# Optimization experiments

Hardware: AMD Instinct MI355X
Metric: run time of the kernel (lower is better)

The kernel has to match this reference:

```python
import jax, jax.numpy as jnp
import numpy as np

N_NODES = 100000
N_EDGES = 1250000
IN_DIM = 6
HID = 64


def gcn_conv(x, W, b, src, dst, deg_inv_sqrt):
    # x: [N, F_in] -> [N, F_out]; symmetric-normalized aggregation with self-loops
    h = x @ W  # [N, F_out]
    norm = deg_inv_sqrt[src] * deg_inv_sqrt[dst]  # [E]
    msg = h[src] * norm[:, None]                  # gather + scale, [E, F_out]
    agg = jax.ops.segment_sum(msg, dst, num_segments=x.shape[0])
    # self-loop contribution: norm = deg_inv_sqrt[i]^2 = 1/deg[i]
    out = agg + h * (deg_inv_sqrt ** 2)[:, None] + b
    return out


def setup_inputs() -> dict:
    key = jax.random.key(0)
    ks = jax.random.split(key, 8)
    x = jax.random.normal(ks[0], (N_NODES, IN_DIM), dtype=jnp.float32)
    edge_index = jax.random.randint(ks[1], (2, N_EDGES), 0, N_NODES, dtype=jnp.int64)
    s1 = 1.0 / np.sqrt(IN_DIM)
    s2 = 1.0 / np.sqrt(HID)
    W1 = jax.random.uniform(ks[2], (IN_DIM, HID), jnp.float32, -s1, s1)
    b1 = jnp.zeros((HID,), jnp.float32)
    W2 = jax.random.uniform(ks[3], (HID, HID), jnp.float32, -s2, s2)
    b2 = jnp.zeros((HID,), jnp.float32)
    Wfc = jax.random.uniform(ks[4], (HID, 1), jnp.float32, -s2, s2)
    bfc = jnp.zeros((1,), jnp.float32)
    return {"x": x, "edge_index": edge_index, "W1": W1, "b1": b1,
            "W2": W2, "b2": b2, "Wfc": Wfc, "bfc": bfc}


def reference(x, edge_index, W1, b1, W2, b2, Wfc, bfc):
    src, dst = edge_index[0], edge_index[1]
    n = x.shape[0]
    # degree with self-loops (GCN default): in-degree at destination + 1
    deg = jax.ops.segment_sum(jnp.ones((src.shape[0],), x.dtype), dst, num_segments=n) + 1.0
    deg_inv_sqrt = jax.lax.rsqrt(deg)
    h = gcn_conv(x, W1, b1, src, dst, deg_inv_sqrt)
    h = jax.nn.relu(h)
    h = gcn_conv(h, W2, b2, src, dst, deg_inv_sqrt)
    g = h.mean(axis=0)              # [HID] graph readout
    out = jax.nn.sigmoid(g @ Wfc + bfc)  # [1]
    return out
```

## Files before the change

### kernel.cpp

```cpp
#include <hip/hip_runtime.h>
#include <math.h>

#define N_NODES 100000
#define N_EDGES 1250000
#define IN_DIM 6
#define HID 64

#define BIN_SHIFT 8
#define BIN_NODES 256
#define NBIN 391
#define A_BLOCKS 250
#define EPB (N_EDGES / A_BLOCKS)
#define CAP 4096
#define SOFF (NBIN * CAP)

__device__ inline float lo16(unsigned u) { return __uint_as_float(u << 16); }
__device__ inline float hi16(unsigned u) { return __uint_as_float(u & 0xffff0000u); }
__device__ inline unsigned short f2bf(float f) {
    unsigned u = __float_as_uint(f);
    u += 0x7FFFu + ((u >> 16) & 1u);
    return (unsigned short)(u >> 16);
}
__device__ inline unsigned pack2(float a, float b) {
    return (unsigned)f2bf(a) | ((unsigned)f2bf(b) << 16);
}

__global__ __launch_bounds__(1024) void binFill(const int* __restrict__ src,
                                                const int* __restrict__ dst,
                                                int* __restrict__ cnt,
                                                unsigned* __restrict__ rec) {
    __shared__ int lc[NBIN];
    __shared__ int scv[NBIN];
    __shared__ int lb[NBIN];
    __shared__ int lbase[NBIN];
    __shared__ unsigned ldsRec[EPB];
    __shared__ int ldsPos[EPB];

    int t = threadIdx.x;
    int base = blockIdx.x * EPB;

    int4 dA = *(const int4*)&dst[base + t * 4];
    int4 sA = *(const int4*)&src[base + t * 4];
    const int TB = (EPB - 4096) / 4;
    bool hasB = (t < TB);
    int4 dB = make_int4(0, 0, 0, 0), sB = make_int4(0, 0, 0, 0);
    if (hasB) {
        dB = *(const int4*)&dst[base + 4096 + t * 4];
        sB = *(const int4*)&src[base + 4096 + t * 4];
    }

#define HIST4(v4) do {                                  \
        atomicAdd(&lc[(v4).x >> BIN_SHIFT], 1);         \
        atomicAdd(&lc[(v4).y >> BIN_SHIFT], 1);         \
        atomicAdd(&lc[(v4).z >> BIN_SHIFT], 1);         \
        atomicAdd(&lc[(v4).w >> BIN_SHIFT], 1);         \
    } while (0)

#define SCAT1(key, val) do {                                                  \
        int b_ = (key) >> BIN_SHIFT;                                          \
        int loc_ = lbase[b_] + atomicAdd(&lc[b_], 1);                         \
        loc_ = min(loc_, EPB - 1);                                            \
        ldsRec[loc_] = ((unsigned)((key) & (BIN_NODES - 1)) << 17)            \
                     | (unsigned)(val);                                       \
        ldsPos[loc_] = lb[b_] + (loc_ - lbase[b_]);                           \
    } while (0)

#define SCAT4(k4, v4) do {                  \
        SCAT1((k4).x, (v4).x);              \
        SCAT1((k4).y, (v4).y);              \
        SCAT1((k4).z, (v4).z);              \
        SCAT1((k4).w, (v4).w);              \
    } while (0)

#define WRITEOUT() do {                                                       \
        for (int i = t; i < EPB; i += 1024) {                                 \
            unsigned p_ = (unsigned)ldsPos[i];                                \
            if (p_ < (unsigned)(2 * SOFF)) rec[p_] = ldsRec[i];               \
        }                                                                     \
    } while (0)

    if (t < NBIN) lc[t] = 0;
    __syncthreads();
    HIST4(dA);
    if (hasB) HIST4(dB);
    __syncthreads();
    if (t < NBIN) {
        int c = lc[t];
        scv[t] = c;
        lc[t] = 0;
        int off = (c > 0) ? atomicAdd(&cnt[t], c) : 0;
        lb[t] = t * CAP + off;
    }
    __syncthreads();
    if (t < 64) {
        int carry = 0;
#pragma unroll
        for (int cb = 0; cb < NBIN; cb += 64) {
            int idx = cb + t;
            int c = (idx < NBIN) ? scv[idx] : 0;
            int v = c;
#pragma unroll
            for (int off = 1; off < 64; off <<= 1) {
                int u = __shfl_up(v, off, 64);
                if (t >= off) v += u;
            }
            if (idx < NBIN) lbase[idx] = carry + v - c;
            carry += __shfl(v, 63, 64);
        }
    }
    __syncthreads();
    SCAT4(dA, sA);
    if (hasB) SCAT4(dB, sB);
    __syncthreads();
    WRITEOUT();
    __syncthreads();

    if (t < NBIN) lc[t] = 0;
    __syncthreads();
    HIST4(sA);
    if (hasB) HIST4(sB);
    __syncthreads();
    if (t < NBIN) {
        int c = lc[t];
        scv[t] = c;
        lc[t] = 0;
        int off = (c > 0) ? atomicAdd(&cnt[NBIN + t], c) : 0;
        lb[t] = SOFF + t * CAP + off;
    }
    __syncthreads();
    if (t < 64) {
        int carry = 0;
#pragma unroll
        for (int cb = 0; cb < NBIN; cb += 64) {
            int idx = cb + t;
            int c = (idx < NBIN) ? scv[idx] : 0;
            int v = c;
#pragma unroll
            for (int off = 1; off < 64; off <<= 1) {
                int u = __shfl_up(v, off, 64);
                if (t >= off) v += u;
            }
            if (idx < NBIN) lbase[idx] = carry + v - c;
            carry += __shfl(v, 63, 64);
        }
    }
    __syncthreads();
    SCAT4(sA, dA);
    if (hasB) SCAT4(sB, dB);
    __syncthreads();
    WRITEOUT();

#undef HIST4
#undef SCAT1
#undef SCAT4
#undef WRITEOUT
}

__global__ __launch_bounds__(1024) void disXH(const unsigned* __restrict__ rec,
                                              const int* __restrict__ cnt,
                                              const float* __restrict__ x,
                                              int* __restrict__ deg,
                                              float* __restrict__ dis,
                                              uint4* __restrict__ xpad) {
    __shared__ int histS[4][BIN_NODES];
    int t = threadIdx.x, g = t >> 8;
    if (t < 4 * BIN_NODES) ((int*)histS)[t] = 0;
    __syncthreads();
    int bin = blockIdx.x;
    int beg = bin * CAP, end = beg + cnt[bin];
    for (int j = beg + t; j < end; j += 1024) atomicAdd(&histS[g][rec[j] >> 17], 1);
    __syncthreads();
    if (t < BIN_NODES) {
        int n = (bin << BIN_SHIFT) + t;
        if (n < N_NODES) {
            int h = histS[0][t] + histS[1][t] + histS[2][t] + histS[3][t];
            deg[n] = h;
            float d = rsqrtf((float)h + 1.0f);
            dis[n] = d;
            float2 xa = *(const float2*)&x[n * IN_DIM + 0];
            float2 xb = *(const float2*)&x[n * IN_DIM + 2];
            float2 xc = *(const float2*)&x[n * IN_DIM + 4];
            uint4 u;
            u.x = pack2(xa.x * d, xa.y * d);
            u.y = pack2(xb.x * d, xb.y * d);
            u.z = pack2(xc.x * d, xc.y * d);
            u.w = 0;
            xpad[n] = u;
        }
    }
}

__global__ __launch_bounds__(1024) void aggW(const unsigned* __restrict__ rec,
                                             const int* __restrict__ cnt,
                                             const int* __restrict__ deg,
                                             const float* __restrict__ dis,
                                             const uint4* __restrict__ xpad,
                                             const float* __restrict__ W1,
                                             const float* __restrict__ b1,
                                             float* __restrict__ vsum) {
    __shared__ unsigned srcL[CAP];
    __shared__ float wlS[4][BIN_NODES];
    __shared__ int degL[BIN_NODES];
    __shared__ int startS[BIN_NODES];
    __shared__ int cur[BIN_NODES];
    __shared__ int sc[BIN_NODES];
    __shared__ float sAll[BIN_NODES][8];
    __shared__ float w1s[IN_DIM * HID];
    __shared__ float b1s[HID];
    __shared__ float vpart[HID];
    int t = threadIdx.x, g = t >> 8;
    int bin = blockIdx.x;

    if (t < 4 * BIN_NODES) ((float*)wlS)[t] = 0.f;
    if (t < IN_DIM * HID) w1s[t] = W1[t];
    if (t >= 1024 - HID) { int c = t - (1024 - HID); b1s[c] = b1[c]; vpart[c] = 0.f; }
    __syncthreads();

    {
        int beg = SOFF + bin * CAP, end = beg + cnt[NBIN + bin];
        for (int j = beg + t; j < end; j += 1024) {
            unsigned r = rec[j];
            atomicAdd(&wlS[g][r >> 17], dis[r & 131071u]);
        }
    }
    __syncthreads();

    if (t < BIN_NODES) {
        int n = (bin << BIN_SHIFT) + t;
        int h = (n < N_NODES) ? deg[n] : 0;
        degL[t] = h;
        sc[t] = h;
        float d = (n < N_NODES) ? rsqrtf((float)h + 1.0f) : 0.f;
        float wloc = wlS[0][t] + wlS[1][t] + wlS[2][t] + wlS[3][t];
        sAll[t][6] = d;
        sAll[t][7] = (n < N_NODES) ? d * (wloc + d) : 0.f;
    }
    __syncthreads();
    for (int off = 1; off < BIN_NODES; off <<= 1) {
        int add = 0;
        if (t < BIN_NODES && t >= off) add = sc[t - off];
        __syncthreads();
        if (t < BIN_NODES) sc[t] += add;
        __syncthreads();
    }
    if (t < BIN_NODES) {
        int st = sc[t] - degL[t];
        startS[t] = st;
        cur[t] = st;
    }
    __syncthreads();

    {
        int beg = bin * CAP, end = beg + cnt[bin];
        for (int j = beg + t; j < end; j += 1024) {
            unsigned r = rec[j];
            int pos = atomicAdd(&cur[r >> 17], 1);
            if (pos < CAP) srcL[pos] = r & 131071u;
        }
    }
    __syncthreads();

    {
        int node = t >> 2, sub = t & 3;
        int st = startS[node], cn = degL[node];
        int lim = min(st + cn, CAP);
        float s0 = 0.f, s1 = 0.f, s2 = 0.f, s3 = 0.f, s4 = 0.f, s5 = 0.f;
        for (int k = st + sub; k < lim; k += 4) {
            uint4 px = xpad[srcL[k]];
            s0 += lo16(px.x); s1 += hi16(px.x);
            s2 += lo16(px.y); s3 += hi16(px.y);
            s4 += lo16(px.z); s5 += hi16(px.z);
        }
        s0 += __shfl_xor(s0, 1, 64); s0 += __shfl_xor(s0, 2, 64);
        s1 += __shfl_xor(s1, 1, 64); s1 += __shfl_xor(s1, 2, 64);
        s2 += __shfl_xor(s2, 1, 64); s2 += __shfl_xor(s2, 2, 64);
        s3 += __shfl_xor(s3, 1, 64); s3 += __shfl_xor(s3, 2, 64);
        s4 += __shfl_xor(s4, 1, 64); s4 += __shfl_xor(s4, 2, 64);
        s5 += __shfl_xor(s5, 1, 64); s5 += __shfl_xor(s5, 2, 64);
        if (sub == 0) {
            int n = (bin << BIN_SHIFT) + node;
            if (n < N_NODES) {
                uint4 px = xpad[n];
                s0 += lo16(px.x); s1 += hi16(px.x);
                s2 += lo16(px.y); s3 += hi16(px.y);
                s4 += lo16(px.z); s5 += hi16(px.z);
            }
            sAll[node][0] = s0; sAll[node][1] = s1; sAll[node][2] = s2;
            sAll[node][3] = s3; sAll[node][4] = s4; sAll[node][5] = s5;
        }
    }
    __syncthreads();

    {
        int c = t & 63, grp = t >> 6;
        float v = 0.f;
#pragma unroll
        for (int i = 0; i < 16; ++i) {
            int node = grp * 16 + i;
            float d = sAll[node][6], cw = sAll[node][7];
            float a = sAll[node][0] * w1s[0 * HID + c]
                    + sAll[node][1] * w1s[1 * HID + c]
                    + sAll[node][2] * w1s[2 * HID + c]
                    + sAll[node][3] * w1s[3 * HID + c]
                    + sAll[node][4] * w1s[4 * HID + c]
                    + sAll[node][5] * w1s[5 * HID + c];
            v += cw * fmaxf(d * a + b1s[c], 0.f);
        }
        atomicAdd(&vpart[c], v);
    }
    __syncthreads();
    if (t < HID) atomicAdd(&vsum[t], vpart[t]);
}

__global__ void finalK(const float* __restrict__ vsum, const float* __restrict__ W2,
                       const float* __restrict__ b2, const float* __restrict__ Wfc,
                       const float* __restrict__ bfc, float* __restrict__ out) {
    __shared__ float vL[HID];
    int t = threadIdx.x;
    vL[t] = vsum[t] * (1.0f / N_NODES);
    __syncthreads();
    float g = b2[t];
    for (int k = 0; k < HID; ++k) g += vL[k] * W2[k * HID + t];
    float z = g * Wfc[t];
    for (int off = 32; off > 0; off >>= 1) z += __shfl_down(z, off, 64);
    if (t == 0) out[0] = 1.0f / (1.0f + expf(-(z + bfc[0])));
}

extern "C" void kernel_launch(void* const* d_in, const int* in_sizes, int n_in,
                              void* d_out, int out_size, void* d_ws, size_t ws_size,
                              hipStream_t stream) {
    const float* x   = (const float*)d_in[0];
    const int*   ei  = (const int*)d_in[1];
    const float* W1  = (const float*)d_in[2];
    const float* b1  = (const float*)d_in[3];
    const float* W2  = (const float*)d_in[4];
    const float* b2  = (const float*)d_in[5];
    const float* Wfc = (const float*)d_in[6];
    const float* bfc = (const float*)d_in[7];
    const int* src = ei;
    const int* dst = ei + N_EDGES;

    char* ws = (char*)d_ws;
    size_t off = 0;
    auto alloc = (+[](char* base, size_t* o, size_t bytes) {
        char* p = base + *o;
        *o += (bytes + 255) & ~(size_t)255;
        return p;
    });
    int*      cnt  = (int*)     alloc(ws, &off, (size_t)2 * NBIN * 4);
    float*    vsum = (float*)   alloc(ws, &off, 64 * 4);
    uint4*    xpad = (uint4*)   alloc(ws, &off, (size_t)N_NODES * 16);
    float*    dis  = (float*)   alloc(ws, &off, (size_t)N_NODES * 4);
    int*      deg  = (int*)     alloc(ws, &off, (size_t)N_NODES * 4);
    unsigned* rec  = (unsigned*)alloc(ws, &off, (size_t)2 * SOFF * 4);

    hipMemsetAsync(cnt, 0, ((size_t)2 * NBIN * 4 + 255 & ~(size_t)255) + 64 * 4, stream);

    binFill<<<A_BLOCKS, 1024, 0, stream>>>(src, dst, cnt, rec);
    disXH<<<NBIN, 1024, 0, stream>>>(rec, cnt, x, deg, dis, xpad);
    aggW<<<NBIN, 1024, 0, stream>>>(rec, cnt, deg, dis, xpad, W1, b1, vsum);
    finalK<<<1, 64, 0, stream>>>(vsum, W2, b2, Wfc, bfc, (float*)d_out);
}
```

Baseline: 124.0 us.

## Drop source-binned edge copy; push-scatter dis weights via global atomics

Removes the second binning pass by source node, which halves the record buffer and skips one histogram, scan, scatter and writeout in binFill. The per-source sum of destination dis values is now computed in the degree kernel: each dst-bin block stages its records in LDS and does a global atomicAdd of dis[dst] into wsum[src]. aggW then reads wsum instead of accumulating it from source-binned records. The trade is about 1.25M scattered global float atomics in place of the LDS-local accumulation, plus a larger memset that now also clears wsum.

```diff
diff --git a/kernel.cpp b/kernel.cpp
--- a/kernel.cpp
+++ b/kernel.cpp
@@ -70,13 +70,6 @@
         SCAT1((k4).y, (v4).y);              \
         SCAT1((k4).z, (v4).z);              \
         SCAT1((k4).w, (v4).w);              \
-    } while (0)
-
-#define WRITEOUT() do {                                                       \
-        for (int i = t; i < EPB; i += 1024) {                                 \
-            unsigned p_ = (unsigned)ldsPos[i];                                \
-            if (p_ < (unsigned)(2 * SOFF)) rec[p_] = ldsRec[i];               \
-        }                                                                     \
     } while (0)
 
     if (t < NBIN) lc[t] = 0;
@@ -112,71 +105,45 @@
     SCAT4(dA, sA);
     if (hasB) SCAT4(dB, sB);
     __syncthreads();
-    WRITEOUT();
-    __syncthreads();
-
-    if (t < NBIN) lc[t] = 0;
-    __syncthreads();
-    HIST4(sA);
-    if (hasB) HIST4(sB);
-    __syncthreads();
-    if (t < NBIN) {
-        int c = lc[t];
-        scv[t] = c;
-        lc[t] = 0;
-        int off = (c > 0) ? atomicAdd(&cnt[NBIN + t], c) : 0;
-        lb[t] = SOFF + t * CAP + off;
-    }
-    __syncthreads();
-    if (t < 64) {
-        int carry = 0;
-#pragma unroll
-        for (int cb = 0; cb < NBIN; cb += 64) {
-            int idx = cb + t;
-            int c = (idx < NBIN) ? scv[idx] : 0;
-            int v = c;
-#pragma unroll
-            for (int off = 1; off < 64; off <<= 1) {
-                int u = __shfl_up(v, off, 64);
-                if (t >= off) v += u;
-            }
-            if (idx < NBIN) lbase[idx] = carry + v - c;
-            carry += __shfl(v, 63, 64);
-        }
-    }
-    __syncthreads();
-    SCAT4(sA, dA);
-    if (hasB) SCAT4(sB, dB);
-    __syncthreads();
-    WRITEOUT();
+    for (int i = t; i < EPB; i += 1024) {
+        unsigned p = (unsigned)ldsPos[i];
+        if (p < (unsigned)SOFF) rec[p] = ldsRec[i];
+    }
 
 #undef HIST4
 #undef SCAT1
 #undef SCAT4
-#undef WRITEOUT
-}
-
-__global__ __launch_bounds__(1024) void disXH(const unsigned* __restrict__ rec,
+}
+
+__global__ __launch_bounds__(1024) void disXS(const unsigned* __restrict__ rec,
                                               const int* __restrict__ cnt,
                                               const float* __restrict__ x,
                                               int* __restrict__ deg,
-                                              float* __restrict__ dis,
-                                              uint4* __restrict__ xpad) {
+                                              uint4* __restrict__ xpad,
+                                              float* __restrict__ wsum) {
+    __shared__ unsigned stage[CAP];
     __shared__ int histS[4][BIN_NODES];
+    __shared__ float disL[BIN_NODES];
     int t = threadIdx.x, g = t >> 8;
     if (t < 4 * BIN_NODES) ((int*)histS)[t] = 0;
     __syncthreads();
     int bin = blockIdx.x;
-    int beg = bin * CAP, end = beg + cnt[bin];
-    for (int j = beg + t; j < end; j += 1024) atomicAdd(&histS[g][rec[j] >> 17], 1);
+    int beg = bin * CAP;
+    int cn = cnt[bin];
+    if (cn > CAP) cn = CAP;
+    for (int j = t; j < cn; j += 1024) {
+        unsigned r = rec[beg + j];
+        stage[j] = r;
+        atomicAdd(&histS[g][r >> 17], 1);
+    }
     __syncthreads();
     if (t < BIN_NODES) {
         int n = (bin << BIN_SHIFT) + t;
+        float d = 0.f;
         if (n < N_NODES) {
             int h = histS[0][t] + histS[1][t] + histS[2][t] + histS[3][t];
             deg[n] = h;
-            float d = rsqrtf((float)h + 1.0f);
-            dis[n] = d;
+            d = rsqrtf((float)h + 1.0f);
             float2 xa = *(const float2*)&x[n * IN_DIM + 0];
             float2 xb = *(const float2*)&x[n * IN_DIM + 2];
             float2 xc = *(const float2*)&x[n * IN_DIM + 4];
@@ -187,19 +154,24 @@
             u.w = 0;
             xpad[n] = u;
         }
+        disL[t] = d;
+    }
+    __syncthreads();
+    for (int j = t; j < cn; j += 1024) {
+        unsigned r = stage[j];
+        atomicAdd(&wsum[r & 131071u], disL[r >> 17]);
     }
 }
 
 __global__ __launch_bounds__(1024) void aggW(const unsigned* __restrict__ rec,
                                              const int* __restrict__ cnt,
                                              const int* __restrict__ deg,
-                                             const float* __restrict__ dis,
+                                             const float* __restrict__ wsum,
                                              const uint4* __restrict__ xpad,
                                              const float* __restrict__ W1,
                                              const float* __restrict__ b1,
                                              float* __restrict__ vsum) {
     __shared__ unsigned srcL[CAP];
-    __shared__ float wlS[4][BIN_NODES];
     __shared__ int degL[BIN_NODES];
     __shared__ int startS[BIN_NODES];
     __shared__ int cur[BIN_NODES];
@@ -208,22 +180,11 @@
     __shared__ float w1s[IN_DIM * HID];
     __shared__ float b1s[HID];
     __shared__ float vpart[HID];
-    int t = threadIdx.x, g = t >> 8;
+    int t = threadIdx.x;
     int bin = blockIdx.x;
 
-    if (t < 4 * BIN_NODES) ((float*)wlS)[t] = 0.f;
     if (t < IN_DIM * HID) w1s[t] = W1[t];
     if (t >= 1024 - HID) { int c = t - (1024 - HID); b1s[c] = b1[c]; vpart[c] = 0.f; }
-    __syncthreads();
-
-    {
-        int beg = SOFF + bin * CAP, end = beg + cnt[NBIN + bin];
-        for (int j = beg + t; j < end; j += 1024) {
-            unsigned r = rec[j];
-            atomicAdd(&wlS[g][r >> 17], dis[r & 131071u]);
-        }
-    }
-    __syncthreads();
 
     if (t < BIN_NODES) {
         int n = (bin << BIN_SHIFT) + t;
@@ -231,7 +192,7 @@
         degL[t] = h;
         sc[t] = h;
         float d = (n < N_NODES) ? rsqrtf((float)h + 1.0f) : 0.f;
-        float wloc = wlS[0][t] + wlS[1][t] + wlS[2][t] + wlS[3][t];
+        float wloc = (n < N_NODES) ? wsum[n] : 0.f;
         sAll[t][6] = d;
         sAll[t][7] = (n < N_NODES) ? d * (wloc + d) : 0.f;
     }
@@ -347,17 +308,17 @@
         *o += (bytes + 255) & ~(size_t)255;
         return p;
     });
-    int*      cnt  = (int*)     alloc(ws, &off, (size_t)2 * NBIN * 4);
+    int*      cnt  = (int*)     alloc(ws, &off, (size_t)NBIN * 4);
     float*    vsum = (float*)   alloc(ws, &off, 64 * 4);
+    float*    wsum = (float*)   alloc(ws, &off, (size_t)N_NODES * 4);
     uint4*    xpad = (uint4*)   alloc(ws, &off, (size_t)N_NODES * 16);
-    float*    dis  = (float*)   alloc(ws, &off, (size_t)N_NODES * 4);
     int*      deg  = (int*)     alloc(ws, &off, (size_t)N_NODES * 4);
-    unsigned* rec  = (unsigned*)alloc(ws, &off, (size_t)2 * SOFF * 4);
-
-    hipMemsetAsync(cnt, 0, ((size_t)2 * NBIN * 4 + 255 & ~(size_t)255) + 64 * 4, stream);
+    unsigned* rec  = (unsigned*)alloc(ws, &off, (size_t)SOFF * 4);
+
+    hipMemsetAsync(cnt, 0, (size_t)((char*)xpad - (char*)cnt), stream);
 
     binFill<<<A_BLOCKS, 1024, 0, stream>>>(src, dst, cnt, rec);
-    disXH<<<NBIN, 1024, 0, stream>>>(rec, cnt, x, deg, dis, xpad);
-    aggW<<<NBIN, 1024, 0, stream>>>(rec, cnt, deg, dis, xpad, W1, b1, vsum);
+    disXS<<<NBIN, 1024, 0, stream>>>(rec, cnt, x, deg, xpad, wsum);
+    aggW<<<NBIN, 1024, 0, stream>>>(rec, cnt, deg, wsum, xpad, W1, b1, vsum);
     finalK<<<1, 64, 0, stream>>>(vsum, W2, b2, Wfc, bfc, (float*)d_out);
 }
```

New measurement: 176.9 us. 42.6% more time.

## Fuse all four kernels into one cooperative persistent kernel with grid syncs

Applied to the files above, without the earlier changes.

Replaces the four separate launches (bin fill, degree/xpad, aggregation, final) with a single cooperative kernel of 256 blocks. The phases are separated by grid.sync, and later phases loop over the 391 bins in a grid-stride loop. Shared memory is overlaid through a union of the per-phase layouts. The aim is to remove the launch gaps and tail idle time between kernels, in exchange for grid-sync overhead, fewer blocks than bins in the bin phases (some blocks handle two bins), and idle blocks during the final step.

```diff
diff --git a/kernel.cpp b/kernel.cpp
--- a/kernel.cpp
+++ b/kernel.cpp
@@ -1,5 +1,8 @@
 #include <hip/hip_runtime.h>
+#include <hip/hip_cooperative_groups.h>
 #include <math.h>
+
+namespace cg = cooperative_groups;
 
 #define N_NODES 100000
 #define N_EDGES 1250000
@@ -13,6 +16,7 @@
 #define EPB (N_EDGES / A_BLOCKS)
 #define CAP 4096
 #define SOFF (NBIN * CAP)
+#define GRID_B 256
 
 __device__ inline float lo16(unsigned u) { return __uint_as_float(u << 16); }
 __device__ inline float hi16(unsigned u) { return __uint_as_float(u & 0xffff0000u); }
@@ -25,305 +29,300 @@
     return (unsigned)f2bf(a) | ((unsigned)f2bf(b) << 16);
 }
 
-__global__ __launch_bounds__(1024) void binFill(const int* __restrict__ src,
-                                                const int* __restrict__ dst,
-                                                int* __restrict__ cnt,
-                                                unsigned* __restrict__ rec) {
-    __shared__ int lc[NBIN];
-    __shared__ int scv[NBIN];
-    __shared__ int lb[NBIN];
-    __shared__ int lbase[NBIN];
-    __shared__ unsigned ldsRec[EPB];
-    __shared__ int ldsPos[EPB];
-
+struct P1 {
+    int lc[NBIN];
+    int scv[NBIN];
+    int lb[NBIN];
+    int lbase[NBIN];
+    unsigned ldsRec[EPB];
+    int ldsPos[EPB];
+};
+struct P23 {
+    unsigned srcL[CAP];
+    union { int hist[4][BIN_NODES]; float wl[4][BIN_NODES]; } h;
+    int degL[BIN_NODES];
+    int startS[BIN_NODES];
+    int cur[BIN_NODES];
+    int sc[BIN_NODES];
+    float sAll[BIN_NODES][8];
+    float w1s[IN_DIM * HID];
+    float b1s[HID];
+    float vpart[HID];
+};
+
+__global__ __launch_bounds__(1024) void fused(
+    const int* __restrict__ src, const int* __restrict__ dst,
+    const float* __restrict__ x,
+    const float* __restrict__ W1, const float* __restrict__ b1,
+    const float* __restrict__ W2, const float* __restrict__ b2,
+    const float* __restrict__ Wfc, const float* __restrict__ bfc,
+    int* __restrict__ cnt, unsigned* __restrict__ rec,
+    int* __restrict__ deg, float* __restrict__ dis,
+    uint4* __restrict__ xpad, float* __restrict__ vsum,
+    float* __restrict__ out)
+{
+    __shared__ union { P1 a; P23 b; } S;
+    cg::grid_group grid = cg::this_grid();
     int t = threadIdx.x;
-    int base = blockIdx.x * EPB;
-
-    int4 dA = *(const int4*)&dst[base + t * 4];
-    int4 sA = *(const int4*)&src[base + t * 4];
-    const int TB = (EPB - 4096) / 4;
-    bool hasB = (t < TB);
-    int4 dB = make_int4(0, 0, 0, 0), sB = make_int4(0, 0, 0, 0);
-    if (hasB) {
-        dB = *(const int4*)&dst[base + 4096 + t * 4];
-        sB = *(const int4*)&src[base + 4096 + t * 4];
-    }
-
-#define HIST4(v4) do {                                  \
-        atomicAdd(&lc[(v4).x >> BIN_SHIFT], 1);         \
-        atomicAdd(&lc[(v4).y >> BIN_SHIFT], 1);         \
-        atomicAdd(&lc[(v4).z >> BIN_SHIFT], 1);         \
-        atomicAdd(&lc[(v4).w >> BIN_SHIFT], 1);         \
-    } while (0)
+
+    if (blockIdx.x < A_BLOCKS) {
+        int base = blockIdx.x * EPB;
+        int4 dA = *(const int4*)&dst[base + t * 4];
+        int4 sA = *(const int4*)&src[base + t * 4];
+        const int TB = (EPB - 4096) / 4;
+        bool hasB = (t < TB);
+        int4 dB = make_int4(0, 0, 0, 0), sB = make_int4(0, 0, 0, 0);
+        if (hasB) {
+            dB = *(const int4*)&dst[base + 4096 + t * 4];
+            sB = *(const int4*)&src[base + 4096 + t * 4];
+        }
+
+#define HIST4(v4) do {                                      \
+            atomicAdd(&S.a.lc[(v4).x >> BIN_SHIFT], 1);     \
+            atomicAdd(&S.a.lc[(v4).y >> BIN_SHIFT], 1);     \
+            atomicAdd(&S.a.lc[(v4).z >> BIN_SHIFT], 1);     \
+            atomicAdd(&S.a.lc[(v4).w >> BIN_SHIFT], 1);     \
+        } while (0)
 
 #define SCAT1(key, val) do {                                                  \
-        int b_ = (key) >> BIN_SHIFT;                                          \
-        int loc_ = lbase[b_] + atomicAdd(&lc[b_], 1);                         \
-        loc_ = min(loc_, EPB - 1);                                            \
-        ldsRec[loc_] = ((unsigned)((key) & (BIN_NODES - 1)) << 17)            \
-                     | (unsigned)(val);                                       \
-        ldsPos[loc_] = lb[b_] + (loc_ - lbase[b_]);                           \
-    } while (0)
+            int b_ = (key) >> BIN_SHIFT;                                      \
+            int loc_ = S.a.lbase[b_] + atomicAdd(&S.a.lc[b_], 1);             \
+            loc_ = min(loc_, EPB - 1);                                        \
+            S.a.ldsRec[loc_] = ((unsigned)((key) & (BIN_NODES - 1)) << 17)    \
+                             | (unsigned)(val);                               \
+            S.a.ldsPos[loc_] = S.a.lb[b_] + (loc_ - S.a.lbase[b_]);           \
+        } while (0)
 
 #define SCAT4(k4, v4) do {                  \
-        SCAT1((k4).x, (v4).x);              \
-        SCAT1((k4).y, (v4).y);              \
-        SCAT1((k4).z, (v4).z);              \
-        SCAT1((k4).w, (v4).w);              \
-    } while (0)
+            SCAT1((k4).x, (v4).x);          \
+            SCAT1((k4).y, (v4).y);          \
+            SCAT1((k4).z, (v4).z);          \
+            SCAT1((k4).w, (v4).w);          \
+        } while (0)
+
+#define WAVE_SCAN() do {                                                      \
+            if (t < 64) {                                                     \
+                int carry = 0;                                                \
+                for (int cb = 0; cb < NBIN; cb += 64) {                       \
+                    int idx = cb + t;                                         \
+                    int c = (idx < NBIN) ? S.a.scv[idx] : 0;                  \
+                    int v = c;                                                \
+                    for (int off = 1; off < 64; off <<= 1) {                  \
+                        int u = __shfl_up(v, off, 64);                        \
+                        if (t >= off) v += u;                                 \
+                    }                                                         \
+                    if (idx < NBIN) S.a.lbase[idx] = carry + v - c;           \
+                    carry += __shfl(v, 63, 64);                               \
+                }                                                             \
+            }                                                                 \
+        } while (0)
 
 #define WRITEOUT() do {                                                       \
-        for (int i = t; i < EPB; i += 1024) {                                 \
-            unsigned p_ = (unsigned)ldsPos[i];                                \
-            if (p_ < (unsigned)(2 * SOFF)) rec[p_] = ldsRec[i];               \
-        }                                                                     \
-    } while (0)
-
-    if (t < NBIN) lc[t] = 0;
-    __syncthreads();
-    HIST4(dA);
-    if (hasB) HIST4(dB);
-    __syncthreads();
-    if (t < NBIN) {
-        int c = lc[t];
-        scv[t] = c;
-        lc[t] = 0;
-        int off = (c > 0) ? atomicAdd(&cnt[t], c) : 0;
-        lb[t] = t * CAP + off;
-    }
-    __syncthreads();
-    if (t < 64) {
-        int carry = 0;
-#pragma unroll
-        for (int cb = 0; cb < NBIN; cb += 64) {
-            int idx = cb + t;
-            int c = (idx < NBIN) ? scv[idx] : 0;
-            int v = c;
-#pragma unroll
-            for (int off = 1; off < 64; off <<= 1) {
-                int u = __shfl_up(v, off, 64);
-                if (t >= off) v += u;
-            }
-            if (idx < NBIN) lbase[idx] = carry + v - c;
-            carry += __shfl(v, 63, 64);
-        }
-    }
-    __syncthreads();
-    SCAT4(dA, sA);
-    if (hasB) SCAT4(dB, sB);
-    __syncthreads();
-    WRITEOUT();
-    __syncthreads();
-
-    if (t < NBIN) lc[t] = 0;
-    __syncthreads();
-    HIST4(sA);
-    if (hasB) HIST4(sB);
-    __syncthreads();
-    if (t < NBIN) {
-        int c = lc[t];
-        scv[t] = c;
-        lc[t] = 0;
-        int off = (c > 0) ? atomicAdd(&cnt[NBIN + t], c) : 0;
-        lb[t] = SOFF + t * CAP + off;
-    }
-    __syncthreads();
-    if (t < 64) {
-        int carry = 0;
-#pragma unroll
-        for (int cb = 0; cb < NBIN; cb += 64) {
-            int idx = cb + t;
-            int c = (idx < NBIN) ? scv[idx] : 0;
-            int v = c;
-#pragma unroll
-            for (int off = 1; off < 64; off <<= 1) {
-                int u = __shfl_up(v, off, 64);
-                if (t >= off) v += u;
-            }
-            if (idx < NBIN) lbase[idx] = carry + v - c;
-            carry += __shfl(v, 63, 64);
-        }
-    }
-    __syncthreads();
-    SCAT4(sA, dA);
-    if (hasB) SCAT4(sB, dB);
-    __syncthreads();
-    WRITEOUT();
+            for (int i = t; i < EPB; i += 1024) {                             \
+                unsigned p_ = (unsigned)S.a.ldsPos[i];                        \
+                if (p_ < (unsigned)(2 * SOFF)) rec[p_] = S.a.ldsRec[i];       \
+            }                                                                 \
+        } while (0)
+
+        if (t < NBIN) S.a.lc[t] = 0;
+        __syncthreads();
+        HIST4(dA);
+        if (hasB) HIST4(dB);
+        __syncthreads();
+        if (t < NBIN) {
+            int c = S.a.lc[t];
+            S.a.scv[t] = c;
+            S.a.lc[t] = 0;
+            int off = (c > 0) ? atomicAdd(&cnt[t], c) : 0;
+            S.a.lb[t] = t * CAP + off;
+        }
+        __syncthreads();
+        WAVE_SCAN();
+        __syncthreads();
+        SCAT4(dA, sA);
+        if (hasB) SCAT4(dB, sB);
+        __syncthreads();
+        WRITEOUT();
+        __syncthreads();
+
+        if (t < NBIN) S.a.lc[t] = 0;
+        __syncthreads();
+        HIST4(sA);
+        if (hasB) HIST4(sB);
+        __syncthreads();
+        if (t < NBIN) {
+            int c = S.a.lc[t];
+            S.a.scv[t] = c;
+            S.a.lc[t] = 0;
+            int off = (c > 0) ? atomicAdd(&cnt[NBIN + t], c) : 0;
+            S.a.lb[t] = SOFF + t * CAP + off;
+        }
+        __syncthreads();
+        WAVE_SCAN();
+        __syncthreads();
+        SCAT4(sA, dA);
+        if (hasB) SCAT4(sB, dB);
+        __syncthreads();
+        WRITEOUT();
 
 #undef HIST4
 #undef SCAT1
 #undef SCAT4
+#undef WAVE_SCAN
 #undef WRITEOUT
-}
-
-__global__ __launch_bounds__(1024) void disXH(const unsigned* __restrict__ rec,
-                                              const int* __restrict__ cnt,
-                                              const float* __restrict__ x,
-                                              int* __restrict__ deg,
-                                              float* __restrict__ dis,
-                                              uint4* __restrict__ xpad) {
-    __shared__ int histS[4][BIN_NODES];
-    int t = threadIdx.x, g = t >> 8;
-    if (t < 4 * BIN_NODES) ((int*)histS)[t] = 0;
-    __syncthreads();
-    int bin = blockIdx.x;
-    int beg = bin * CAP, end = beg + cnt[bin];
-    for (int j = beg + t; j < end; j += 1024) atomicAdd(&histS[g][rec[j] >> 17], 1);
-    __syncthreads();
-    if (t < BIN_NODES) {
-        int n = (bin << BIN_SHIFT) + t;
-        if (n < N_NODES) {
-            int h = histS[0][t] + histS[1][t] + histS[2][t] + histS[3][t];
-            deg[n] = h;
-            float d = rsqrtf((float)h + 1.0f);
-            dis[n] = d;
-            float2 xa = *(const float2*)&x[n * IN_DIM + 0];
-            float2 xb = *(const float2*)&x[n * IN_DIM + 2];
-            float2 xc = *(const float2*)&x[n * IN_DIM + 4];
-            uint4 u;
-            u.x = pack2(xa.x * d, xa.y * d);
-            u.y = pack2(xb.x * d, xb.y * d);
-            u.z = pack2(xc.x * d, xc.y * d);
-            u.w = 0;
-            xpad[n] = u;
-        }
-    }
-}
-
-__global__ __launch_bounds__(1024) void aggW(const unsigned* __restrict__ rec,
-                                             const int* __restrict__ cnt,
-                                             const int* __restrict__ deg,
-                                             const float* __restrict__ dis,
-                                             const uint4* __restrict__ xpad,
-                                             const float* __restrict__ W1,
-                                             const float* __restrict__ b1,
-                                             float* __restrict__ vsum) {
-    __shared__ unsigned srcL[CAP];
-    __shared__ float wlS[4][BIN_NODES];
-    __shared__ int degL[BIN_NODES];
-    __shared__ int startS[BIN_NODES];
-    __shared__ int cur[BIN_NODES];
-    __shared__ int sc[BIN_NODES];
-    __shared__ float sAll[BIN_NODES][8];
-    __shared__ float w1s[IN_DIM * HID];
-    __shared__ float b1s[HID];
-    __shared__ float vpart[HID];
-    int t = threadIdx.x, g = t >> 8;
-    int bin = blockIdx.x;
-
-    if (t < 4 * BIN_NODES) ((float*)wlS)[t] = 0.f;
-    if (t < IN_DIM * HID) w1s[t] = W1[t];
-    if (t >= 1024 - HID) { int c = t - (1024 - HID); b1s[c] = b1[c]; vpart[c] = 0.f; }
-    __syncthreads();
-
-    {
-        int beg = SOFF + bin * CAP, end = beg + cnt[NBIN + bin];
-        for (int j = beg + t; j < end; j += 1024) {
-            unsigned r = rec[j];
-            atomicAdd(&wlS[g][r >> 17], dis[r & 131071u]);
-        }
-    }
-    __syncthreads();
-
-    if (t < BIN_NODES) {
-        int n = (bin << BIN_SHIFT) + t;
-        int h = (n < N_NODES) ? deg[n] : 0;
-        degL[t] = h;
-        sc[t] = h;
-        float d = (n < N_NODES) ? rsqrtf((float)h + 1.0f) : 0.f;
-        float wloc = wlS[0][t] + wlS[1][t] + wlS[2][t] + wlS[3][t];
-        sAll[t][6] = d;
-        sAll[t][7] = (n < N_NODES) ? d * (wloc + d) : 0.f;
-    }
-    __syncthreads();
-    for (int off = 1; off < BIN_NODES; off <<= 1) {
-        int add = 0;
-        if (t < BIN_NODES && t >= off) add = sc[t - off];
-        __syncthreads();
-        if (t < BIN_NODES) sc[t] += add;
-        __syncthreads();
-    }
-    if (t < BIN_NODES) {
-        int st = sc[t] - degL[t];
-        startS[t] = st;
-        cur[t] = st;
-    }
-    __syncthreads();
-
-    {
-        int beg = bin * CAP, end = beg + cnt[bin];
-        for (int j = beg + t; j < end; j += 1024) {
-            unsigned r = rec[j];
-            int pos = atomicAdd(&cur[r >> 17], 1);
-            if (pos < CAP) srcL[pos] = r & 131071u;
-        }
-    }
-    __syncthreads();
-
-    {
-        int node = t >> 2, sub = t & 3;
-        int st = startS[node], cn = degL[node];
-        int lim = min(st + cn, CAP);
-        float s0 = 0.f, s1 = 0.f, s2 = 0.f, s3 = 0.f, s4 = 0.f, s5 = 0.f;
-        for (int k = st + sub; k < lim; k += 4) {
-            uint4 px = xpad[srcL[k]];
-            s0 += lo16(px.x); s1 += hi16(px.x);
-            s2 += lo16(px.y); s3 += hi16(px.y);
-            s4 += lo16(px.z); s5 += hi16(px.z);
-        }
-        s0 += __shfl_xor(s0, 1, 64); s0 += __shfl_xor(s0, 2, 64);
-        s1 += __shfl_xor(s1, 1, 64); s1 += __shfl_xor(s1, 2, 64);
-        s2 += __shfl_xor(s2, 1, 64); s2 += __shfl_xor(s2, 2, 64);
-        s3 += __shfl_xor(s3, 1, 64); s3 += __shfl_xor(s3, 2, 64);
-        s4 += __shfl_xor(s4, 1, 64); s4 += __shfl_xor(s4, 2, 64);
-        s5 += __shfl_xor(s5, 1, 64); s5 += __shfl_xor(s5, 2, 64);
-        if (sub == 0) {
-            int n = (bin << BIN_SHIFT) + node;
+    }
+    grid.sync();
+
+    if (t < IN_DIM * HID) S.b.w1s[t] = W1[t];
+    if (t >= 1024 - HID) {
+        int c = t - (1024 - HID);
+        S.b.b1s[c] = b1[c];
+        S.b.vpart[c] = 0.f;
+    }
+
+    for (int bin = (int)blockIdx.x; bin < NBIN; bin += GRID_B) {
+        if (t < 4 * BIN_NODES) ((int*)S.b.h.hist)[t] = 0;
+        __syncthreads();
+        int beg = bin * CAP;
+        int cn = cnt[bin]; if (cn > CAP) cn = CAP;
+        int g = t >> 8;
+        for (int j = t; j < cn; j += 1024)
+            atomicAdd(&S.b.h.hist[g][rec[beg + j] >> 17], 1);
+        __syncthreads();
+        if (t < BIN_NODES) {
+            int n = (bin << BIN_SHIFT) + t;
             if (n < N_NODES) {
-                uint4 px = xpad[n];
+                int h = S.b.h.hist[0][t] + S.b.h.hist[1][t]
+                      + S.b.h.hist[2][t] + S.b.h.hist[3][t];
+                deg[n] = h;
+                float d = rsqrtf((float)h + 1.0f);
+                dis[n] = d;
+                float2 xa = *(const float2*)&x[n * IN_DIM + 0];
+                float2 xb = *(const float2*)&x[n * IN_DIM + 2];
+                float2 xc = *(const float2*)&x[n * IN_DIM + 4];
+                uint4 u;
+                u.x = pack2(xa.x * d, xa.y * d);
+                u.y = pack2(xb.x * d, xb.y * d);
+                u.z = pack2(xc.x * d, xc.y * d);
+                u.w = 0;
+                xpad[n] = u;
+            }
+        }
+        __syncthreads();
+    }
+    grid.sync();
+
+    for (int bin = (int)blockIdx.x; bin < NBIN; bin += GRID_B) {
+        if (t < 4 * BIN_NODES) ((float*)S.b.h.wl)[t] = 0.f;
+        __syncthreads();
+        {
+            int beg2 = SOFF + bin * CAP;
+            int cn2 = cnt[NBIN + bin]; if (cn2 > CAP) cn2 = CAP;
+            int g = t >> 8;
+            for (int j = t; j < cn2; j += 1024) {
+                unsigned r = rec[beg2 + j];
+                atomicAdd(&S.b.h.wl[g][r >> 17], dis[r & 131071u]);
+            }
+        }
+        __syncthreads();
+        if (t < BIN_NODES) {
+            int n = (bin << BIN_SHIFT) + t;
+            int h = (n < N_NODES) ? deg[n] : 0;
+            S.b.degL[t] = h;
+            S.b.sc[t] = h;
+            float d = (n < N_NODES) ? rsqrtf((float)h + 1.0f) : 0.f;
+            float wloc = S.b.h.wl[0][t] + S.b.h.wl[1][t]
+                       + S.b.h.wl[2][t] + S.b.h.wl[3][t];
+            S.b.sAll[t][6] = d;
+            S.b.sAll[t][7] = (n < N_NODES) ? d * (wloc + d) : 0.f;
+        }
+        __syncthreads();
+        for (int off = 1; off < BIN_NODES; off <<= 1) {
+            int add = 0;
+            if (t < BIN_NODES && t >= off) add = S.b.sc[t - off];
+            __syncthreads();
+            if (t < BIN_NODES) S.b.sc[t] += add;
+            __syncthreads();
+        }
+        if (t < BIN_NODES) {
+            int st = S.b.sc[t] - S.b.degL[t];
+            S.b.startS[t] = st;
+            S.b.cur[t] = st;
+        }
+        __syncthreads();
+        {
+            int beg = bin * CAP;
+            int cn = cnt[bin]; if (cn > CAP) cn = CAP;
+            for (int j = t; j < cn; j += 1024) {
+                unsigned r = rec[beg + j];
+                int pos = atomicAdd(&S.b.cur[r >> 17], 1);
+                if (pos < CAP) S.b.srcL[pos] = r & 131071u;
+            }
+        }
+        __syncthreads();
+        {
+            int node = t >> 2, sub = t & 3;
+            int st = S.b.startS[node], cnD = S.b.degL[node];
+            int lim = min(st + cnD, CAP);
+            float s0 = 0.f, s1 = 0.f, s2 = 0.f, s3 = 0.f, s4 = 0.f, s5 = 0.f;
+            for (int k = st + sub; k < lim; k += 4) {
+                uint4 px = xpad[S.b.srcL[k]];
                 s0 += lo16(px.x); s1 += hi16(px.x);
                 s2 += lo16(px.y); s3 += hi16(px.y);
                 s4 += lo16(px.z); s5 += hi16(px.z);
             }
-            sAll[node][0] = s0; sAll[node][1] = s1; sAll[node][2] = s2;
-            sAll[node][3] = s3; sAll[node][4] = s4; sAll[node][5] = s5;
-        }
-    }
-    __syncthreads();
-
-    {
-        int c = t & 63, grp = t >> 6;
-        float v = 0.f;
+            s0 += __shfl_xor(s0, 1, 64); s0 += __shfl_xor(s0, 2, 64);
+            s1 += __shfl_xor(s1, 1, 64); s1 += __shfl_xor(s1, 2, 64);
+            s2 += __shfl_xor(s2, 1, 64); s2 += __shfl_xor(s2, 2, 64);
+            s3 += __shfl_xor(s3, 1, 64); s3 += __shfl_xor(s3, 2, 64);
+            s4 += __shfl_xor(s4, 1, 64); s4 += __shfl_xor(s4, 2, 64);
+            s5 += __shfl_xor(s5, 1, 64); s5 += __shfl_xor(s5, 2, 64);
+            if (sub == 0) {
+                int n = (bin << BIN_SHIFT) + node;
+                if (n < N_NODES) {
+                    uint4 px = xpad[n];
+                    s0 += lo16(px.x); s1 += hi16(px.x);
+                    s2 += lo16(px.y); s3 += hi16(px.y);
+                    s4 += lo16(px.z); s5 += hi16(px.z);
+                }
+                S.b.sAll[node][0] = s0; S.b.sAll[node][1] = s1;
+                S.b.sAll[node][2] = s2; S.b.sAll[node][3] = s3;
+                S.b.sAll[node][4] = s4; S.b.sAll[node][5] = s5;
+            }
+        }
+        __syncthreads();
+        {
+            int c = t & 63, grp = t >> 6;
+            float v = 0.f;
 #pragma unroll
-        for (int i = 0; i < 16; ++i) {
-            int node = grp * 16 + i;
-            float d = sAll[node][6], cw = sAll[node][7];
-            float a = sAll[node][0] * w1s[0 * HID + c]
-                    + sAll[node][1] * w1s[1 * HID + c]
-                    + sAll[node][2] * w1s[2 * HID + c]
-                    + sAll[node][3] * w1s[3 * HID + c]
-                    + sAll[node][4] * w1s[4 * HID + c]
-                    + sAll[node][5] * w1s[5 * HID + c];
-            v += cw * fmaxf(d * a + b1s[c], 0.f);
-        }
-        atomicAdd(&vpart[c], v);
-    }
-    __syncthreads();
-    if (t < HID) atomicAdd(&vsum[t], vpart[t]);
-}
-
-__global__ void finalK(const float* __restrict__ vsum, const float* __restrict__ W2,
-                       const float* __restrict__ b2, const float* __restrict__ Wfc,
-                       const float* __restrict__ bfc, float* __restrict__ out) {
-    __shared__ float vL[HID];
-    int t = threadIdx.x;
-    vL[t] = vsum[t] * (1.0f / N_NODES);
-    __syncthreads();
-    float g = b2[t];
-    for (int k = 0; k < HID; ++k) g += vL[k] * W2[k * HID + t];
-    float z = g * Wfc[t];
-    for (int off = 32; off > 0; off >>= 1) z += __shfl_down(z, off, 64);
-    if (t == 0) out[0] = 1.0f / (1.0f + expf(-(z + bfc[0])));
+            for (int i = 0; i < 16; ++i) {
+                int node = grp * 16 + i;
+                float d = S.b.sAll[node][6], cw = S.b.sAll[node][7];
+                float a = S.b.sAll[node][0] * S.b.w1s[0 * HID + c]
+                        + S.b.sAll[node][1] * S.b.w1s[1 * HID + c]
+                        + S.b.sAll[node][2] * S.b.w1s[2 * HID + c]
+                        + S.b.sAll[node][3] * S.b.w1s[3 * HID + c]
+                        + S.b.sAll[node][4] * S.b.w1s[4 * HID + c]
+                        + S.b.sAll[node][5] * S.b.w1s[5 * HID + c];
+                v += cw * fmaxf(d * a + S.b.b1s[c], 0.f);
+            }
+            atomicAdd(&S.b.vpart[c], v);
+        }
+        __syncthreads();
+    }
+    if (t < HID) atomicAdd(&vsum[t], S.b.vpart[t]);
+    grid.sync();
+
+    if (blockIdx.x == 0 && t < 64) {
+        float vv = vsum[t] * (1.0f / N_NODES);
+        float gacc = b2[t];
+#pragma unroll 8
+        for (int k = 0; k < HID; ++k)
+            gacc += __shfl(vv, k, 64) * W2[k * HID + t];
+        float z = gacc * Wfc[t];
+        for (int off = 32; off > 0; off >>= 1) z += __shfl_down(z, off, 64);
+        if (t == 0) out[0] = 1.0f / (1.0f + expf(-(z + bfc[0])));
+    }
 }
 
 extern "C" void kernel_launch(void* const* d_in, const int* in_sizes, int n_in,
@@ -349,15 +348,21 @@
     });
     int*      cnt  = (int*)     alloc(ws, &off, (size_t)2 * NBIN * 4);
     float*    vsum = (float*)   alloc(ws, &off, 64 * 4);
+    int*      deg  = (int*)     alloc(ws, &off, (size_t)N_NODES * 4);
+    float*    dis  = (float*)   alloc(ws, &off, (size_t)N_NODES * 4);
     uint4*    xpad = (uint4*)   alloc(ws, &off, (size_t)N_NODES * 16);
-    float*    dis  = (float*)   alloc(ws, &off, (size_t)N_NODES * 4);
-    int*      deg  = (int*)     alloc(ws, &off, (size_t)N_NODES * 4);
     unsigned* rec  = (unsigned*)alloc(ws, &off, (size_t)2 * SOFF * 4);
 
-    hipMemsetAsync(cnt, 0, ((size_t)2 * NBIN * 4 + 255 & ~(size_t)255) + 64 * 4, stream);
-
-    binFill<<<A_BLOCKS, 1024, 0, stream>>>(src, dst, cnt, rec);
-    disXH<<<NBIN, 1024, 0, stream>>>(rec, cnt, x, deg, dis, xpad);
-    aggW<<<NBIN, 1024, 0, stream>>>(rec, cnt, deg, dis, xpad, W1, b1, vsum);
-    finalK<<<1, 64, 0, stream>>>(vsum, W2, b2, Wfc, bfc, (float*)d_out);
+    hipMemsetAsync(cnt, 0, (size_t)((char*)deg - (char*)cnt), stream);
+
+    float* outp = (float*)d_out;
+    void* args[] = {
+        (void*)&src, (void*)&dst, (void*)&x,
+        (void*)&W1, (void*)&b1, (void*)&W2, (void*)&b2,
+        (void*)&Wfc, (void*)&bfc,
+        (void*)&cnt, (void*)&rec, (void*)&deg, (void*)&dis,
+        (void*)&xpad, (void*)&vsum, (void*)&outp
+    };
+    hipLaunchCooperativeKernel((void*)fused, dim3(GRID_B), dim3(1024),
+                               args, 0, stream);
 }
```

Measured after the change: 242.4 us. 95.4% more time.

## Halve block size of disXH/aggW and use wave-level shuffle scan for offsets

Applied to the files above, without the earlier changes.

Reduces disXH and aggW from 1024 to 512 threads per block, with 2 histogram copies instead of 4 and 2 lanes per node instead of 4 in the gather. The 256-entry prefix scan of node degrees moves from a shared-memory scan with many __syncthreads to a single wavefront doing __shfl_up scans in four 64-wide chunks. Bin counts are clamped to CAP and the workspace buffers are reordered so the memset size is computed from pointers. The aim is lower barrier cost and smaller blocks so more blocks fit per CU, at the cost of fewer threads per bin.

```diff
diff --git a/kernel.cpp b/kernel.cpp
--- a/kernel.cpp
+++ b/kernel.cpp
@@ -156,24 +156,25 @@
 #undef WRITEOUT
 }
 
-__global__ __launch_bounds__(1024) void disXH(const unsigned* __restrict__ rec,
-                                              const int* __restrict__ cnt,
-                                              const float* __restrict__ x,
-                                              int* __restrict__ deg,
-                                              float* __restrict__ dis,
-                                              uint4* __restrict__ xpad) {
-    __shared__ int histS[4][BIN_NODES];
+__global__ __launch_bounds__(512) void disXH(const unsigned* __restrict__ rec,
+                                             const int* __restrict__ cnt,
+                                             const float* __restrict__ x,
+                                             int* __restrict__ deg,
+                                             float* __restrict__ dis,
+                                             uint4* __restrict__ xpad) {
+    __shared__ int histS[2][BIN_NODES];
     int t = threadIdx.x, g = t >> 8;
-    if (t < 4 * BIN_NODES) ((int*)histS)[t] = 0;
+    if (t < 2 * BIN_NODES) ((int*)histS)[t] = 0;
     __syncthreads();
     int bin = blockIdx.x;
-    int beg = bin * CAP, end = beg + cnt[bin];
-    for (int j = beg + t; j < end; j += 1024) atomicAdd(&histS[g][rec[j] >> 17], 1);
+    int beg = bin * CAP;
+    int cn = cnt[bin]; if (cn > CAP) cn = CAP;
+    for (int j = t; j < cn; j += 512) atomicAdd(&histS[g][rec[beg + j] >> 17], 1);
     __syncthreads();
     if (t < BIN_NODES) {
         int n = (bin << BIN_SHIFT) + t;
         if (n < N_NODES) {
-            int h = histS[0][t] + histS[1][t] + histS[2][t] + histS[3][t];
+            int h = histS[0][t] + histS[1][t];
             deg[n] = h;
             float d = rsqrtf((float)h + 1.0f);
             dis[n] = d;
@@ -190,20 +191,19 @@
     }
 }
 
-__global__ __launch_bounds__(1024) void aggW(const unsigned* __restrict__ rec,
-                                             const int* __restrict__ cnt,
-                                             const int* __restrict__ deg,
-                                             const float* __restrict__ dis,
-                                             const uint4* __restrict__ xpad,
-                                             const float* __restrict__ W1,
-                                             const float* __restrict__ b1,
-                                             float* __restrict__ vsum) {
+__global__ __launch_bounds__(512) void aggW(const unsigned* __restrict__ rec,
+                                            const int* __restrict__ cnt,
+                                            const int* __restrict__ deg,
+                                            const float* __restrict__ dis,
+                                            const uint4* __restrict__ xpad,
+                                            const float* __restrict__ W1,
+                                            const float* __restrict__ b1,
+                                            float* __restrict__ vsum) {
     __shared__ unsigned srcL[CAP];
-    __shared__ float wlS[4][BIN_NODES];
+    __shared__ float wlS[2][BIN_NODES];
     __shared__ int degL[BIN_NODES];
     __shared__ int startS[BIN_NODES];
     __shared__ int cur[BIN_NODES];
-    __shared__ int sc[BIN_NODES];
     __shared__ float sAll[BIN_NODES][8];
     __shared__ float w1s[IN_DIM * HID];
     __shared__ float b1s[HID];
@@ -211,15 +211,16 @@
     int t = threadIdx.x, g = t >> 8;
     int bin = blockIdx.x;
 
-    if (t < 4 * BIN_NODES) ((float*)wlS)[t] = 0.f;
+    if (t < 2 * BIN_NODES) ((float*)wlS)[t] = 0.f;
     if (t < IN_DIM * HID) w1s[t] = W1[t];
-    if (t >= 1024 - HID) { int c = t - (1024 - HID); b1s[c] = b1[c]; vpart[c] = 0.f; }
+    if (t >= 512 - HID) { int c = t - (512 - HID); b1s[c] = b1[c]; vpart[c] = 0.f; }
     __syncthreads();
 
     {
-        int beg = SOFF + bin * CAP, end = beg + cnt[NBIN + bin];
-        for (int j = beg + t; j < end; j += 1024) {
-            unsigned r = rec[j];
+        int beg = SOFF + bin * CAP;
+        int cn = cnt[NBIN + bin]; if (cn > CAP) cn = CAP;
+        for (int j = t; j < cn; j += 512) {
+            unsigned r = rec[beg + j];
             atomicAdd(&wlS[g][r >> 17], dis[r & 131071u]);
         }
     }
@@ -229,31 +230,37 @@
         int n = (bin << BIN_SHIFT) + t;
         int h = (n < N_NODES) ? deg[n] : 0;
         degL[t] = h;
-        sc[t] = h;
         float d = (n < N_NODES) ? rsqrtf((float)h + 1.0f) : 0.f;
-        float wloc = wlS[0][t] + wlS[1][t] + wlS[2][t] + wlS[3][t];
+        float wloc = wlS[0][t] + wlS[1][t];
         sAll[t][6] = d;
         sAll[t][7] = (n < N_NODES) ? d * (wloc + d) : 0.f;
     }
     __syncthreads();
-    for (int off = 1; off < BIN_NODES; off <<= 1) {
-        int add = 0;
-        if (t < BIN_NODES && t >= off) add = sc[t - off];
-        __syncthreads();
-        if (t < BIN_NODES) sc[t] += add;
-        __syncthreads();
-    }
-    if (t < BIN_NODES) {
-        int st = sc[t] - degL[t];
-        startS[t] = st;
-        cur[t] = st;
+    if (t < 64) {
+        int carry = 0;
+#pragma unroll
+        for (int cb = 0; cb < BIN_NODES; cb += 64) {
+            int idx = cb + t;
+            int c = degL[idx];
+            int v = c;
+#pragma unroll
+            for (int off = 1; off < 64; off <<= 1) {
+                int u = __shfl_up(v, off, 64);
+                if (t >= off) v += u;
+            }
+            int st = carry + v - c;
+            startS[idx] = st;
+            cur[idx] = st;
+            carry += __shfl(v, 63, 64);
+        }
     }
     __syncthreads();
 
     {
-        int beg = bin * CAP, end = beg + cnt[bin];
-        for (int j = beg + t; j < end; j += 1024) {
-            unsigned r = rec[j];
+        int beg = bin * CAP;
+        int cn = cnt[bin]; if (cn > CAP) cn = CAP;
+        for (int j = t; j < cn; j += 512) {
+            unsigned r = rec[beg + j];
             int pos = atomicAdd(&cur[r >> 17], 1);
             if (pos < CAP) srcL[pos] = r & 131071u;
         }
@@ -261,22 +268,22 @@
     __syncthreads();
 
     {
-        int node = t >> 2, sub = t & 3;
+        int node = t >> 1, sub = t & 1;
         int st = startS[node], cn = degL[node];
         int lim = min(st + cn, CAP);
         float s0 = 0.f, s1 = 0.f, s2 = 0.f, s3 = 0.f, s4 = 0.f, s5 = 0.f;
-        for (int k = st + sub; k < lim; k += 4) {
+        for (int k = st + sub; k < lim; k += 2) {
             uint4 px = xpad[srcL[k]];
             s0 += lo16(px.x); s1 += hi16(px.x);
             s2 += lo16(px.y); s3 += hi16(px.y);
             s4 += lo16(px.z); s5 += hi16(px.z);
         }
-        s0 += __shfl_xor(s0, 1, 64); s0 += __shfl_xor(s0, 2, 64);
-        s1 += __shfl_xor(s1, 1, 64); s1 += __shfl_xor(s1, 2, 64);
-        s2 += __shfl_xor(s2, 1, 64); s2 += __shfl_xor(s2, 2, 64);
-        s3 += __shfl_xor(s3, 1, 64); s3 += __shfl_xor(s3, 2, 64);
-        s4 += __shfl_xor(s4, 1, 64); s4 += __shfl_xor(s4, 2, 64);
-        s5 += __shfl_xor(s5, 1, 64); s5 += __shfl_xor(s5, 2, 64);
+        s0 += __shfl_xor(s0, 1, 64);
+        s1 += __shfl_xor(s1, 1, 64);
+        s2 += __shfl_xor(s2, 1, 64);
+        s3 += __shfl_xor(s3, 1, 64);
+        s4 += __shfl_xor(s4, 1, 64);
+        s5 += __shfl_xor(s5, 1, 64);
         if (sub == 0) {
             int n = (bin << BIN_SHIFT) + node;
             if (n < N_NODES) {
@@ -295,8 +302,8 @@
         int c = t & 63, grp = t >> 6;
         float v = 0.f;
 #pragma unroll
-        for (int i = 0; i < 16; ++i) {
-            int node = grp * 16 + i;
+        for (int i = 0; i < 32; ++i) {
+            int node = grp * 32 + i;
             float d = sAll[node][6], cw = sAll[node][7];
             float a = sAll[node][0] * w1s[0 * HID + c]
                     + sAll[node][1] * w1s[1 * HID + c]
@@ -349,15 +356,15 @@
     });
     int*      cnt  = (int*)     alloc(ws, &off, (size_t)2 * NBIN * 4);
     float*    vsum = (float*)   alloc(ws, &off, 64 * 4);
+    int*      deg  = (int*)     alloc(ws, &off, (size_t)N_NODES * 4);
+    float*    dis  = (float*)   alloc(ws, &off, (size_t)N_NODES * 4);
     uint4*    xpad = (uint4*)   alloc(ws, &off, (size_t)N_NODES * 16);
-    float*    dis  = (float*)   alloc(ws, &off, (size_t)N_NODES * 4);
-    int*      deg  = (int*)     alloc(ws, &off, (size_t)N_NODES * 4);
     unsigned* rec  = (unsigned*)alloc(ws, &off, (size_t)2 * SOFF * 4);
 
-    hipMemsetAsync(cnt, 0, ((size_t)2 * NBIN * 4 + 255 & ~(size_t)255) + 64 * 4, stream);
+    hipMemsetAsync(cnt, 0, (size_t)((char*)deg - (char*)cnt), stream);
 
     binFill<<<A_BLOCKS, 1024, 0, stream>>>(src, dst, cnt, rec);
-    disXH<<<NBIN, 1024, 0, stream>>>(rec, cnt, x, deg, dis, xpad);
-    aggW<<<NBIN, 1024, 0, stream>>>(rec, cnt, deg, dis, xpad, W1, b1, vsum);
+    disXH<<<NBIN, 512, 0, stream>>>(rec, cnt, x, deg, dis, xpad);
+    aggW<<<NBIN, 512, 0, stream>>>(rec, cnt, deg, dis, xpad, W1, b1, vsum);
     finalK<<<1, 64, 0, stream>>>(vsum, W2, b2, Wfc, bfc, (float*)d_out);
 }
```

New measurement: 126.8 us. +2.3%, slower.
